# Kernel tuning notes

Hardware: AMD Instinct MI355X
Metric: run time of the kernel (lower is better)

## Reference

```python
import jax, jax.numpy as jnp
import numpy as np
from jax import lax

NUM_HEADS = 4
DIM = 192
EPS = 1e-12  # torch F.normalize eps


def setup_inputs() -> dict:
    key = jax.random.key(0)
    ks = jax.random.split(key, 5)
    b, c, h, w = 8, DIM, 128, 128
    x = jax.random.normal(ks[0], (b, c, h, w), dtype=jnp.float32)
    f = jax.random.normal(ks[1], (b, c, h, w), dtype=jnp.float32)
    # conv weights, scaled like kaiming-ish init
    w_qkv = jax.random.normal(ks[2], (3 * c, c, 1, 1), dtype=jnp.float32) * (1.0 / np.sqrt(c))
    w_dw = jax.random.normal(ks[3], (3 * c, 1, 3, 3), dtype=jnp.float32) * (1.0 / 3.0)
    w_proj = jax.random.normal(ks[4], (c, c, 1, 1), dtype=jnp.float32) * (1.0 / np.sqrt(c))
    temperature = jnp.ones((NUM_HEADS, 1, 1), dtype=jnp.float32)
    return {"x": x, "f": f, "w_qkv": w_qkv, "w_dw": w_dw, "w_proj": w_proj,
            "temperature": temperature}


def _conv(x, w, groups=1):
    return lax.conv_general_dilated(
        x, w, window_strides=(1, 1), padding="SAME",
        dimension_numbers=("NCHW", "OIHW", "NCHW"),
        feature_group_count=groups)


def reference(x, f, w_qkv, w_dw, w_proj, temperature):
    b, c, h, w = x.shape
    x_in = x + f
    qkv = _conv(x_in, w_qkv)                 # [b, 3c, h, w] 1x1 conv
    qkv = _conv(qkv, w_dw, groups=3 * c)     # depthwise 3x3
    q, k, v = jnp.split(qkv, 3, axis=1)      # each [b, c, h, w]
    hw = h * w
    ch = c // NUM_HEADS

    def heads(t):
        return t.reshape(b, NUM_HEADS, ch, hw)  # 'b (head c) h w -> b head c (h w)'

    q, k, v = heads(q), heads(k), heads(v)
    # L2-normalize over spatial (last) dim, torch-style eps clamp
    q = q / jnp.maximum(jnp.linalg.norm(q, axis=-1, keepdims=True), EPS)
    k = k / jnp.maximum(jnp.linalg.norm(k, axis=-1, keepdims=True), EPS)
    # transposed (channel) attention: [b, head, ch, ch]
    attn = jnp.einsum("bhcn,bhdn->bhcd", q, k) * temperature[None]
    attn = jax.nn.softmax(attn, axis=-1)
    out = jnp.einsum("bhcd,bhdn->bhcn", attn, v)  # [b, head, ch, hw]
    out = out.reshape(b, c, h, w)
    return _conv(out, w_proj)
```

## Files before the change

kernel.cpp:

```cpp
#include <hip/hip_runtime.h>
#include <stdint.h>

#define NB 8
#define NC 192
#define NOC 576
#define NH 4
#define HW 16384
#define NCHUNK 16

typedef unsigned short u16;
typedef __bf16 v8bf __attribute__((ext_vector_type(8)));
typedef float v4f __attribute__((ext_vector_type(4)));
typedef u16 v8us __attribute__((ext_vector_type(8)));
typedef u16 v4us __attribute__((ext_vector_type(4)));

__device__ __forceinline__ u16 f2bf(float f) {
    uint32_t u = __float_as_uint(f);
    u += 0x7FFFu + ((u >> 16) & 1u);
    return (u16)(u >> 16);
}
__device__ __forceinline__ float bf2f(u16 u) {
    return __uint_as_float(((uint32_t)u) << 16);
}

__global__ void k_cvt_w(const float* __restrict__ w, u16* __restrict__ wb, int n) {
    int i = blockIdx.x * 256 + threadIdx.x;
    if (i < n) wb[i] = f2bf(w[i]);
}

__global__ __launch_bounds__(1024) void k_gemm_qkv(
    const float* __restrict__ x, const float* __restrict__ f,
    const u16* __restrict__ wb, u16* __restrict__ qkv, int b0)
{
    __shared__ u16 smem[43008];
    u16* bt = smem;
    u16* wt = smem + 24576;
    const int t = threadIdx.x;
    const int bl = blockIdx.y;
    const int bg = b0 + bl;
    const int p0 = blockIdx.x * 128;

    {
        const int px = t & 127;
        const int cg = t >> 7;
        #pragma unroll
        for (int it = 0; it < 3; ++it) {
            const int c4 = it * 8 + cg;
            const size_t base = ((size_t)bg * NC + c4 * 8) * HW + p0 + px;
            v8us pk;
            #pragma unroll
            for (int j = 0; j < 8; ++j) {
                float v = x[base + (size_t)j * HW] + f[base + (size_t)j * HW];
                pk[j] = f2bf(v);
            }
            *reinterpret_cast<v8us*>(&bt[px * 192 + ((c4 ^ (px & 7)) << 3)]) = pk;
        }
    }

    const int w = t >> 6, l = t & 63, lr = l & 15, lg = l >> 4;
    const int wp = w >> 2;
    const int wo = w & 3;
    const int oc0 = wo * 144;

    v4f acc[2][9];
    #pragma unroll
    for (int mi = 0; mi < 2; ++mi)
        #pragma unroll
        for (int ni = 0; ni < 9; ++ni)
            acc[mi][ni] = (v4f){0.f, 0.f, 0.f, 0.f};

    v8us wload[3];
    #pragma unroll
    for (int it = 0; it < 3; ++it) {
        const int idx = it * 1024 + t;
        if (idx < 2304) {
            const int oc = idx >> 2, q = idx & 3;
            wload[it] = *reinterpret_cast<const v8us*>(&wb[oc * 192 + q * 8]);
        }
    }

    #pragma unroll 1
    for (int ks = 0; ks < 6; ++ks) {
        __syncthreads();
        #pragma unroll
        for (int it = 0; it < 3; ++it) {
            const int idx = it * 1024 + t;
            if (idx < 2304) {
                const int oc = idx >> 2, q = idx & 3;
                const int g = (oc ^ (oc >> 2)) & 3;
                *reinterpret_cast<v8us*>(&wt[oc * 32 + ((q ^ g) << 3)]) = wload[it];
            }
        }
        if (ks < 5) {
            #pragma unroll
            for (int it = 0; it < 3; ++it) {
                const int idx = it * 1024 + t;
                if (idx < 2304) {
                    const int oc = idx >> 2, q = idx & 3;
                    wload[it] = *reinterpret_cast<const v8us*>(&wb[oc * 192 + (ks + 1) * 32 + q * 8]);
                }
            }
        }
        __syncthreads();

        v8bf a[2];
        #pragma unroll
        for (int mi = 0; mi < 2; ++mi) {
            const int px = wp * 32 + mi * 16 + lr;
            a[mi] = *reinterpret_cast<const v8bf*>(&bt[px * 192 + (((ks * 4 + lg) ^ (px & 7)) << 3)]);
        }
        #pragma unroll
        for (int ni = 0; ni < 9; ++ni) {
            const int oc = oc0 + ni * 16 + lr;
            const int g = (oc ^ (oc >> 2)) & 3;
            const v8bf bw = *reinterpret_cast<const v8bf*>(&wt[oc * 32 + ((lg ^ g) << 3)]);
            #pragma unroll
            for (int mi = 0; mi < 2; ++mi)
                acc[mi][ni] = __builtin_amdgcn_mfma_f32_16x16x32_bf16(a[mi], bw, acc[mi][ni], 0, 0, 0);
        }
    }

    u16* et = smem;
    #pragma unroll
    for (int pass = 0; pass < 2; ++pass) {
        __syncthreads();
        if ((wp >> 1) == pass) {
            #pragma unroll
            for (int mi = 0; mi < 2; ++mi)
                #pragma unroll
                for (int ni = 0; ni < 9; ++ni) {
                    const int oc = oc0 + ni * 16 + lr;
                    const int u = (wp & 1) * 8 + mi * 4 + lg;
                    const int su = u ^ (oc & 15);
                    v4us pk;
                    pk[0] = f2bf(acc[mi][ni][0]); pk[1] = f2bf(acc[mi][ni][1]);
                    pk[2] = f2bf(acc[mi][ni][2]); pk[3] = f2bf(acc[mi][ni][3]);
                    *reinterpret_cast<v4us*>(&et[oc * 64 + su * 4]) = pk;
                }
        }
        __syncthreads();
        const size_t obase = ((size_t)bl * 256 + blockIdx.x * 2 + pass) * 36864;
        #pragma unroll
        for (int rd = 0; rd < 5; ++rd) {
            const int idx = rd * 1024 + t;
            if (idx < 4608) {
                const int oc = idx >> 3;
                const int ck = idx & 7;
                const int u0 = (ck * 2) ^ (oc & 15);
                const int u1 = (ck * 2 + 1) ^ (oc & 15);
                v4us lo = *reinterpret_cast<v4us*>(&et[oc * 64 + u0 * 4]);
                v4us hi = *reinterpret_cast<v4us*>(&et[oc * 64 + u1 * 4]);
                v8us o8;
                o8[0] = lo[0]; o8[1] = lo[1]; o8[2] = lo[2]; o8[3] = lo[3];
                o8[4] = hi[0]; o8[5] = hi[1]; o8[6] = hi[2]; o8[7] = hi[3];
                *reinterpret_cast<v8us*>(&qkv[obase + (size_t)idx * 8]) = o8;
            }
        }
    }
}

__global__ __launch_bounds__(512) void k_dw(
    const u16* __restrict__ qkv, const float* __restrict__ wdw,
    u16* __restrict__ qk_out, u16* __restrict__ v_out,
    float* __restrict__ sumsq, int b0)
{
    __shared__ u16 plane[128 * 136];
    __shared__ float red[8];
    const int t = threadIdx.x;
    const int ch = blockIdx.x;
    const int bl = blockIdx.y;
    const int bg = b0 + bl;

    float wk[9];
    #pragma unroll
    for (int i = 0; i < 9; ++i) wk[i] = wdw[ch * 9 + i];

    const int r = t >> 2;
    const int cq = (t & 3) * 32;

    {
        const u16* src = qkv + ((size_t)bl * 256) * 36864 + (size_t)ch * 64;
        #pragma unroll
        for (int i = 0; i < 4; ++i) {
            const int e = i * 4096 + t * 8;
            const int pblk = e >> 6, px = e & 63;
            v8us v = *reinterpret_cast<const v8us*>(&src[(size_t)pblk * 36864 + px]);
            const int rr = e >> 7, cc = e & 127;
            *reinterpret_cast<v8us*>(&plane[rr * 136 + cc]) = v;
        }
    }
    __syncthreads();

    const bool vm = (r > 0), vp = (r < 127);
    const u16* rowm = &plane[(r - 1) * 136];
    const u16* rowc = &plane[r * 136];
    const u16* rowp = &plane[(r + 1) * 136];

    float am, ac, bm, bc, cm, cc2;
    if (cq == 0) { am = 0.f; bm = 0.f; cm = 0.f; }
    else {
        am = vm ? bf2f(rowm[cq - 1]) : 0.f;
        bm = bf2f(rowc[cq - 1]);
        cm = vp ? bf2f(rowp[cq - 1]) : 0.f;
    }
    ac = vm ? bf2f(rowm[cq]) : 0.f;
    bc = bf2f(rowc[cq]);
    cc2 = vp ? bf2f(rowp[cq]) : 0.f;

    uint32_t ov[16];
    float ssq = 0.f;
    #pragma unroll
    for (int xp = 0; xp < 16; ++xp) {
        #pragma unroll
        for (int s2 = 0; s2 < 2; ++s2) {
            const int col = cq + xp * 2 + s2;
            float ap, bp, cp;
            if (col < 127) {
                ap = vm ? bf2f(rowm[col + 1]) : 0.f;
                bp = bf2f(rowc[col + 1]);
                cp = vp ? bf2f(rowp[col + 1]) : 0.f;
            } else { ap = 0.f; bp = 0.f; cp = 0.f; }
            float o = wk[0]*am + wk[1]*ac + wk[2]*ap
                    + wk[3]*bm + wk[4]*bc + wk[5]*bp
                    + wk[6]*cm + wk[7]*cc2 + wk[8]*cp;
            u16 ob = f2bf(o);
            float orr = bf2f(ob);
            ssq += orr * orr;
            ov[xp] = (s2 == 0) ? (uint32_t)ob : (ov[xp] | ((uint32_t)ob << 16));
            am = ac; ac = ap; bm = bc; bc = bp; cm = cc2; cc2 = cp;
        }
    }

    __syncthreads();
    #pragma unroll
    for (int k = 0; k < 4; ++k) {
        uint4 w4;
        w4.x = ov[k * 4 + 0]; w4.y = ov[k * 4 + 1];
        w4.z = ov[k * 4 + 2]; w4.w = ov[k * 4 + 3];
        *reinterpret_cast<uint4*>(&plane[r * 136 + cq + k * 8]) = w4;
    }
    __syncthreads();

    u16* dst = (ch < 2 * NC) ? (qk_out + ((size_t)bg * (2 * NC) + ch) * HW)
                             : (v_out + ((size_t)bg * NC + (ch - 2 * NC)) * HW);
    #pragma unroll
    for (int i = 0; i < 4; ++i) {
        const int idx = i * 4096 + t * 8;
        const int rr = idx >> 7, cc = idx & 127;
        v8us v = *reinterpret_cast<const v8us*>(&plane[rr * 136 + cc]);
        *reinterpret_cast<v8us*>(&dst[idx]) = v;
    }

    #pragma unroll
    for (int off = 32; off > 0; off >>= 1) ssq += __shfl_down(ssq, off);
    if ((t & 63) == 0) red[t >> 6] = ssq;
    __syncthreads();
    if (t == 0 && ch < 2 * NC) {
        float s = 0.f;
        #pragma unroll
        for (int i = 0; i < 8; ++i) s += red[i];
        sumsq[bg * (2 * NC) + ch] = s;
    }
}

__global__ __launch_bounds__(256) void k_attn(
    const u16* __restrict__ qk, float* __restrict__ partials)
{
    __shared__ float wsum[4 * 2304];
    const int t = threadIdx.x;
    const int chunk = blockIdx.x;
    const int h = blockIdx.y;
    const int b = blockIdx.z;
    const int w = t >> 6, l = t & 63, lr = l & 15, lg = l >> 4;

    const size_t qbase = ((size_t)b * 384 + h * 48) * HW;
    const size_t kbase = ((size_t)b * 384 + 192 + h * 48) * HW;
    const int pb = chunk * 1024 + w * 256;

    v4f acc[3][3];
    #pragma unroll
    for (int mi = 0; mi < 3; ++mi)
        #pragma unroll
        for (int ni = 0; ni < 3; ++ni)
            acc[mi][ni] = (v4f){0.f, 0.f, 0.f, 0.f};

    #pragma unroll
    for (int ks = 0; ks < 8; ++ks) {
        const int k = pb + ks * 32 + lg * 8;
        v8bf a[3], bb[3];
        #pragma unroll
        for (int mi = 0; mi < 3; ++mi)
            a[mi] = *reinterpret_cast<const v8bf*>(&qk[qbase + (size_t)(mi * 16 + lr) * HW + k]);
        #pragma unroll
        for (int ni = 0; ni < 3; ++ni)
            bb[ni] = *reinterpret_cast<const v8bf*>(&qk[kbase + (size_t)(ni * 16 + lr) * HW + k]);
        #pragma unroll
        for (int mi = 0; mi < 3; ++mi)
            #pragma unroll
            for (int ni = 0; ni < 3; ++ni)
                acc[mi][ni] = __builtin_amdgcn_mfma_f32_16x16x32_bf16(a[mi], bb[ni], acc[mi][ni], 0, 0, 0);
    }

    #pragma unroll
    for (int mi = 0; mi < 3; ++mi)
        #pragma unroll
        for (int ni = 0; ni < 3; ++ni)
            #pragma unroll
            for (int r = 0; r < 4; ++r)
                wsum[w * 2304 + (mi * 16 + lg * 4 + r) * 48 + ni * 16 + lr] = acc[mi][ni][r];
    __syncthreads();

    #pragma unroll
    for (int i = 0; i < 9; ++i) {
        const int e = t + i * 256;
        float s = wsum[e] + wsum[2304 + e] + wsum[4608 + e] + wsum[6912 + e];
        partials[(((size_t)(b * NH + h)) * NCHUNK + chunk) * 2304 + e] = s;
    }
}

__global__ __launch_bounds__(256) void k_smx(
    const float* __restrict__ partials, const float* __restrict__ sumsq,
    const float* __restrict__ wproj, const float* __restrict__ temp,
    u16* __restrict__ Mb)
{
    __shared__ float att[2304];
    __shared__ float rq[48], rk[48];
    const int t = threadIdx.x;
    const int h = blockIdx.x;
    const int b = blockIdx.y;

    if (t < 48) {
        float s = sumsq[b * 384 + h * 48 + t];
        rq[t] = 1.f / fmaxf(sqrtf(s), 1e-12f);
    } else if (t < 96) {
        float s = sumsq[b * 384 + 192 + h * 48 + (t - 48)];
        rk[t - 48] = 1.f / fmaxf(sqrtf(s), 1e-12f);
    }
    __syncthreads();
    const float tp = temp[h];
    #pragma unroll
    for (int i = 0; i < 9; ++i) {
        const int e = t + i * 256;
        const float* pp = &partials[(((size_t)(b * NH + h)) * NCHUNK) * 2304 + e];
        float s = 0.f;
        #pragma unroll
        for (int c = 0; c < NCHUNK; ++c) s += pp[(size_t)c * 2304];
        att[e] = s * rq[e / 48] * rk[e % 48] * tp;
    }
    __syncthreads();
    if (t < 48) {
        float m = -1e30f;
        #pragma unroll
        for (int j = 0; j < 48; ++j) m = fmaxf(m, att[t * 48 + j]);
        float s = 0.f;
        for (int j = 0; j < 48; ++j) { float e2 = __expf(att[t * 48 + j] - m); att[t * 48 + j] = e2; s += e2; }
        const float inv = 1.f / s;
        for (int j = 0; j < 48; ++j) att[t * 48 + j] *= inv;
    }
    __syncthreads();
    #pragma unroll
    for (int i = 0; i < 36; ++i) {
        const int idx = t + i * 256;
        const int oc = idx / 48, d = idx % 48;
        float s = 0.f;
        #pragma unroll
        for (int cc = 0; cc < 48; ++cc)
            s += wproj[oc * 192 + h * 48 + cc] * att[cc * 48 + d];
        Mb[((size_t)b * NC + oc) * NC + h * 48 + d] = f2bf(s);
    }
}

__global__ __launch_bounds__(256) void k_gemm_out(
    const u16* __restrict__ vp, const u16* __restrict__ Mb,
    float* __restrict__ out)
{
    __shared__ float smemf[12288];
    u16* bt = reinterpret_cast<u16*>(smemf);
    const int t = threadIdx.x;
    const int b = blockIdx.y;
    const int p0 = blockIdx.x * 64;

    {
        const int px = t & 63;
        const int cg = t >> 6;
        #pragma unroll
        for (int it = 0; it < 6; ++it) {
            const int c4 = it * 4 + cg;
            const size_t base = ((size_t)b * NC + c4 * 8) * HW + p0 + px;
            v8us pk;
            #pragma unroll
            for (int j = 0; j < 8; ++j) pk[j] = vp[base + (size_t)j * HW];
            *reinterpret_cast<v8us*>(&bt[px * 192 + ((c4 ^ (px & 7)) << 3)]) = pk;
        }
    }
    __syncthreads();

    const int w = t >> 6, l = t & 63, lr = l & 15, lg = l >> 4;
    const int oc0 = w * 48;

    v4f acc[4][3];
    #pragma unroll
    for (int mi = 0; mi < 4; ++mi)
        #pragma unroll
        for (int ni = 0; ni < 3; ++ni)
            acc[mi][ni] = (v4f){0.f, 0.f, 0.f, 0.f};

    #pragma unroll
    for (int ks = 0; ks < 6; ++ks) {
        const int k = ks * 32 + lg * 8;
        const int c4 = ks * 4 + lg;
        v8bf a[4];
        #pragma unroll
        for (int mi = 0; mi < 4; ++mi) {
            const int px = mi * 16 + lr;
            a[mi] = *reinterpret_cast<const v8bf*>(&bt[px * 192 + ((c4 ^ (px & 7)) << 3)]);
        }
        #pragma unroll
        for (int ni = 0; ni < 3; ++ni) {
            const int oc = oc0 + ni * 16 + lr;
            const v8bf bw = *reinterpret_cast<const v8bf*>(&Mb[((size_t)b * NC + oc) * NC + k]);
            #pragma unroll
            for (int mi = 0; mi < 4; ++mi)
                acc[mi][ni] = __builtin_amdgcn_mfma_f32_16x16x32_bf16(a[mi], bw, acc[mi][ni], 0, 0, 0);
        }
    }

    __syncthreads();
    float* et = smemf;
    #pragma unroll
    for (int mi = 0; mi < 4; ++mi)
        #pragma unroll
        for (int ni = 0; ni < 3; ++ni) {
            const int oc = oc0 + ni * 16 + lr;
            const int u = mi * 4 + lg;
            const int su = u ^ (oc & 15);
            *reinterpret_cast<v4f*>(&et[oc * 64 + su * 4]) = acc[mi][ni];
        }
    __syncthreads();
    #pragma unroll
    for (int rd = 0; rd < 12; ++rd) {
        const int idx = rd * 256 + t;
        const int oc = idx >> 4;
        const int u = idx & 15;
        const int su = u ^ (oc & 15);
        v4f v = *reinterpret_cast<v4f*>(&et[oc * 64 + su * 4]);
        *reinterpret_cast<v4f*>(&out[((size_t)b * NC + oc) * HW + p0 + u * 4]) = v;
    }
}

extern "C" void kernel_launch(void* const* d_in, const int* in_sizes, int n_in,
                              void* d_out, int out_size, void* d_ws, size_t ws_size,
                              hipStream_t stream)
{
    (void)in_sizes; (void)n_in; (void)out_size;
    const float* x      = (const float*)d_in[0];
    const float* f      = (const float*)d_in[1];
    const float* w_qkv  = (const float*)d_in[2];
    const float* w_dw   = (const float*)d_in[3];
    const float* w_proj = (const float*)d_in[4];
    const float* temp   = (const float*)d_in[5];

    char* ws = (char*)d_ws;
    u16*   vws      = (u16*)(ws);
    u16*   wb       = (u16*)(ws + 50331648);
    float* sumsq    = (float*)(ws + 50552832);
    float* partials = (float*)(ws + 50565120);
    u16*   Mb       = (u16*)(ws + 55283712);
    const size_t FIXED = 55873536;
    const size_t PERB  = (size_t)NOC * HW * 2;
    u16*   qkv_raw  = (u16*)(ws + FIXED);

    int g = 1;
    if (ws_size > FIXED + PERB) {
        size_t avail = (ws_size - FIXED) / PERB;
        g = (int)(avail > 8 ? 8 : avail);
        if (g < 1) g = 1;
    }

    u16* qk_scratch = (u16*)d_out;
    float* out      = (float*)d_out;

    hipLaunchKernelGGL(k_cvt_w, dim3(432), dim3(256), 0, stream, w_qkv, wb, NOC * NC);
    for (int b0 = 0; b0 < NB; b0 += g) {
        const int nb = (b0 + g <= NB) ? g : (NB - b0);
        hipLaunchKernelGGL(k_gemm_qkv, dim3(HW / 128, nb), dim3(1024), 0, stream, x, f, wb, qkv_raw, b0);
        hipLaunchKernelGGL(k_dw, dim3(NOC, nb), dim3(512), 0, stream, qkv_raw, w_dw, qk_scratch, vws, sumsq, b0);
    }
    hipLaunchKernelGGL(k_attn, dim3(NCHUNK, NH, NB), dim3(256), 0, stream, qk_scratch, partials);
    hipLaunchKernelGGL(k_smx, dim3(NH, NB), dim3(256), 0, stream, partials, sumsq, w_proj, temp, Mb);
    hipLaunchKernelGGL(k_gemm_out, dim3(HW / 64, NB), dim3(256), 0, stream, vws, Mb, out);
}
```

Measured before the change: 285.2 us.

## Store q/k/v intermediates in row-group-blocked layout for contiguous chunk access

The depthwise-conv kernel now writes q, k and v in a blocked layout of 8-row groups (1024 pixels) per channel, grouped per batch and row-group, instead of one full plane per channel. The attention and output GEMM kernels are updated to read from this layout, so each chunk's channel slices sit close together in memory. This is meant to improve DRAM page and cache locality and reduce strided accesses across 32KB channel planes. It adds more complex indexing and a branch inside the store loop.

```diff
diff --git a/kernel.cpp b/kernel.cpp
--- a/kernel.cpp
+++ b/kernel.cpp
@@ -7,6 +7,7 @@
 #define NH 4
 #define HW 16384
 #define NCHUNK 16
+#define NRG 16
 
 typedef unsigned short u16;
 typedef __bf16 v8bf __attribute__((ext_vector_type(8)));
@@ -241,14 +242,19 @@
     }
     __syncthreads();
 
-    u16* dst = (ch < 2 * NC) ? (qk_out + ((size_t)bg * (2 * NC) + ch) * HW)
-                             : (v_out + ((size_t)bg * NC + (ch - 2 * NC)) * HW);
     #pragma unroll
     for (int i = 0; i < 4; ++i) {
         const int idx = i * 4096 + t * 8;
         const int rr = idx >> 7, cc = idx & 127;
+        const int rg = rr >> 3, rl = rr & 7;
         v8us v = *reinterpret_cast<const v8us*>(&plane[rr * 136 + cc]);
-        *reinterpret_cast<v8us*>(&dst[idx]) = v;
+        if (ch < 2 * NC) {
+            u16* dst = qk_out + (((size_t)(bg * NRG + rg)) * 384 + ch) * 1024 + rl * 128 + cc;
+            *reinterpret_cast<v8us*>(dst) = v;
+        } else {
+            u16* dst = v_out + (((size_t)(bg * NRG + rg)) * 192 + (ch - 384)) * 1024 + rl * 128 + cc;
+            *reinterpret_cast<v8us*>(dst) = v;
+        }
     }
 
     #pragma unroll
@@ -273,9 +279,9 @@
     const int b = blockIdx.z;
     const int w = t >> 6, l = t & 63, lr = l & 15, lg = l >> 4;
 
-    const size_t qbase = ((size_t)b * 384 + h * 48) * HW;
-    const size_t kbase = ((size_t)b * 384 + 192 + h * 48) * HW;
-    const int pb = chunk * 1024 + w * 256;
+    const size_t qbase = ((size_t)(b * NRG + chunk) * 384 + h * 48) * 1024;
+    const size_t kbase = ((size_t)(b * NRG + chunk) * 384 + 192 + h * 48) * 1024;
+    const int pb = w * 256;
 
     v4f acc[3][3];
     #pragma unroll
@@ -290,10 +296,10 @@
         v8bf a[3], bb[3];
         #pragma unroll
         for (int mi = 0; mi < 3; ++mi)
-            a[mi] = *reinterpret_cast<const v8bf*>(&qk[qbase + (size_t)(mi * 16 + lr) * HW + k]);
+            a[mi] = *reinterpret_cast<const v8bf*>(&qk[qbase + (size_t)(mi * 16 + lr) * 1024 + k]);
         #pragma unroll
         for (int ni = 0; ni < 3; ++ni)
-            bb[ni] = *reinterpret_cast<const v8bf*>(&qk[kbase + (size_t)(ni * 16 + lr) * HW + k]);
+            bb[ni] = *reinterpret_cast<const v8bf*>(&qk[kbase + (size_t)(ni * 16 + lr) * 1024 + k]);
         #pragma unroll
         for (int mi = 0; mi < 3; ++mi)
             #pragma unroll
@@ -379,6 +385,7 @@
     const int t = threadIdx.x;
     const int b = blockIdx.y;
     const int p0 = blockIdx.x * 64;
+    const int row = p0 >> 7, rgo = row >> 3, rl = row & 7, c0 = p0 & 127;
 
     {
         const int px = t & 63;
@@ -386,10 +393,10 @@
         #pragma unroll
         for (int it = 0; it < 6; ++it) {
             const int c4 = it * 4 + cg;
-            const size_t base = ((size_t)b * NC + c4 * 8) * HW + p0 + px;
             v8us pk;
             #pragma unroll
-            for (int j = 0; j < 8; ++j) pk[j] = vp[base + (size_t)j * HW];
+            for (int j = 0; j < 8; ++j)
+                pk[j] = vp[((size_t)(b * NRG + rgo) * 192 + c4 * 8 + j) * 1024 + rl * 128 + c0 + px];
             *reinterpret_cast<v8us*>(&bt[px * 192 + ((c4 ^ (px & 7)) << 3)]) = pk;
         }
     }
@@ -477,16 +484,16 @@
         if (g < 1) g = 1;
     }
 
-    u16* qk_scratch = (u16*)d_out;
-    float* out      = (float*)d_out;
+    u16* qk_t = (u16*)d_out;
+    float* out = (float*)d_out;
 
     hipLaunchKernelGGL(k_cvt_w, dim3(432), dim3(256), 0, stream, w_qkv, wb, NOC * NC);
     for (int b0 = 0; b0 < NB; b0 += g) {
         const int nb = (b0 + g <= NB) ? g : (NB - b0);
         hipLaunchKernelGGL(k_gemm_qkv, dim3(HW / 128, nb), dim3(1024), 0, stream, x, f, wb, qkv_raw, b0);
-        hipLaunchKernelGGL(k_dw, dim3(NOC, nb), dim3(512), 0, stream, qkv_raw, w_dw, qk_scratch, vws, sumsq, b0);
-    }
-    hipLaunchKernelGGL(k_attn, dim3(NCHUNK, NH, NB), dim3(256), 0, stream, qk_scratch, partials);
+        hipLaunchKernelGGL(k_dw, dim3(NOC, nb), dim3(512), 0, stream, qkv_raw, w_dw, qk_t, vws, sumsq, b0);
+    }
+    hipLaunchKernelGGL(k_attn, dim3(NCHUNK, NH, NB), dim3(256), 0, stream, qk_t, partials);
     hipLaunchKernelGGL(k_smx, dim3(NH, NB), dim3(256), 0, stream, partials, sumsq, w_proj, temp, Mb);
     hipLaunchKernelGGL(k_gemm_out, dim3(HW / 64, NB), dim3(256), 0, stream, vws, Mb, out);
 }
```

Result: no change. 285.9 us, median of 2 (+0.3%).
